# Kernel optimization log

Hardware: AMD Instinct MI355X
Metric: run time of the kernel (lower is better)

Reference implementation:

```python
import jax, jax.numpy as jnp
import numpy as np

CHUNK = 64
L2_EPS = 1e-6
RMS_EPS = 1e-5


def _silu(x):
    return x * jax.nn.sigmoid(x)


def _causal_shared_conv(x, w):
    # x: [B,T,C]; w: [K] single kernel shared across all channels (depthwise).
    K = w.shape[0]
    T = x.shape[1]
    xp = jnp.pad(x, ((0, 0), (K - 1, 0), (0, 0)))
    out = w[0] * xp[:, 0:T, :]
    for j in range(1, K):  # K=4, tiny fixed loop
        out = out + w[j] * xp[:, j:j + T, :]
    return out


def _l2norm(x):
    return x * jax.lax.rsqrt(jnp.sum(x * x, axis=-1, keepdims=True) + L2_EPS)


def _delta_rule_chunk(q, k, v, beta, chunk=CHUNK):
    # q,k: [B,H,T,dk]; v: [B,H,T,dv]; beta: [B,H,T]
    B, H, T, dk = q.shape
    dv = v.shape[-1]
    q = q * (dk ** -0.5)
    nC = T // chunk
    q = q.reshape(B, H, nC, chunk, dk)
    k = k.reshape(B, H, nC, chunk, dk)
    v = v.reshape(B, H, nC, chunk, dv)
    beta = beta.reshape(B, H, nC, chunk)
    k_beta = k * beta[..., None]
    v_beta = v * beta[..., None]
    # UT transform: invert the unit-lower-triangular (I + stril(K_beta K^T))
    A = jnp.einsum('bhncd,bhnmd->bhncm', k_beta, k)  # [B,H,nC,C,C]
    stril = jnp.tril(jnp.ones((chunk, chunk), bool), -1)
    M = jnp.where(stril, A, 0.0) + jnp.eye(chunk, dtype=q.dtype)
    u = jax.scipy.linalg.solve_triangular(M, v_beta, lower=True)  # T @ (beta*v)
    w = jax.scipy.linalg.solve_triangular(M, k_beta, lower=True)  # T @ (beta*k)
    tril_incl = jnp.tril(jnp.ones((chunk, chunk), bool))

    def step(S, inp):
        q_i, k_i, u_i, w_i = inp  # [B,H,C,d*]
        u_i = u_i - jnp.einsum('bhcd,bhde->bhce', w_i, S)
        attn = jnp.where(tril_incl, jnp.einsum('bhcd,bhmd->bhcm', q_i, k_i), 0.0)
        o_i = jnp.einsum('bhcd,bhde->bhce', q_i, S) + jnp.einsum('bhcm,bhme->bhce', attn, u_i)
        S = S + jnp.einsum('bhcd,bhce->bhde', k_i, u_i)
        return S, o_i

    xs = tuple(jnp.moveaxis(t, 2, 0) for t in (q, k, u, w))
    S0 = jnp.zeros((B, H, dk, dv), q.dtype)
    _, o = jax.lax.scan(step, S0, xs)  # o: [nC,B,H,C,dv]
    return jnp.moveaxis(o, 0, 2).reshape(B, H, T, dv)


def setup_inputs() -> dict:
    key = jax.random.key(0)
    ks = jax.random.split(key, 10)
    B, T, D, H = 2, 4096, 2048, 16
    sc = 0.02
    return {
        'x': jax.random.normal(ks[0], (B, T, D), jnp.float32),
        'Wq': jax.random.normal(ks[1], (D, D), jnp.float32) * sc,
        'Wk': jax.random.normal(ks[2], (D, D), jnp.float32) * sc,
        'Wv': jax.random.normal(ks[3], (D, D), jnp.float32) * sc,
        'Wb': jax.random.normal(ks[4], (D, H), jnp.float32) * sc,
        'Wo': jax.random.normal(ks[5], (D, D), jnp.float32) * sc,
        'conv_q': jax.random.normal(ks[6], (4,), jnp.float32) * 0.5,
        'conv_k': jax.random.normal(ks[7], (4,), jnp.float32) * 0.5,
        'conv_v': jax.random.normal(ks[8], (4,), jnp.float32) * 0.5,
        'onorm_w': jnp.ones((D // H,), jnp.float32),
    }


def reference(x, Wq, Wk, Wv, Wb, Wo, conv_q, conv_k, conv_v, onorm_w):
    B, T, D = x.shape
    H = Wb.shape[1]
    dk = Wq.shape[1] // H
    dv = Wv.shape[1] // H
    # projections + shared-kernel causal short conv (silu activation)
    q = _silu(_causal_shared_conv(x @ Wq, conv_q))
    k = _silu(_causal_shared_conv(x @ Wk, conv_k))
    v = _silu(_causal_shared_conv(x @ Wv, conv_v))
    beta = jax.nn.sigmoid(x @ Wb)  # [B,T,H]
    # split heads -> [B,H,T,d]
    qh = _l2norm(q.reshape(B, T, H, dk)).transpose(0, 2, 1, 3)
    kh = _l2norm(k.reshape(B, T, H, dk)).transpose(0, 2, 1, 3)
    vh = v.reshape(B, T, H, dv).transpose(0, 2, 1, 3)
    o = _delta_rule_chunk(qh, kh, vh, beta.transpose(0, 2, 1))  # [B,H,T,dv]
    o = o.transpose(0, 2, 1, 3)  # [B,T,H,dv]
    # per-head RMSNorm over head_v_dim
    o = o * jax.lax.rsqrt(jnp.mean(o * o, axis=-1, keepdims=True) + RMS_EPS) * onorm_w
    return o.reshape(B, T, H * dv) @ Wo
```

## Files before the change

### kernel.cpp

```cpp
#include <hip/hip_runtime.h>
#include <math.h>

#define B_ 2
#define T_ 4096
#define D_ 2048
#define H_ 16
#define DK 128
#define DV 128
#define CH 64
#define M_ (B_ * T_)
#define NCH (T_ / CH)

typedef __attribute__((ext_vector_type(8))) short bfrag;
typedef __attribute__((ext_vector_type(4))) float ffrag;
typedef __attribute__((ext_vector_type(8))) unsigned short u16x8;
typedef unsigned short us;

#define MFMA __builtin_amdgcn_mfma_f32_16x16x32_bf16

__device__ inline us f2bf(float f) {
  union { float f; unsigned u; } v; v.f = f;
  unsigned r = v.u + 0x7fffu + ((v.u >> 16) & 1u);
  return (us)(r >> 16);
}
__device__ inline float bf2f(us u) {
  union { unsigned u; float f; } v; v.u = ((unsigned)u) << 16;
  return v.f;
}

__device__ inline void gl_lds16(const us* g, us* l) {
  __builtin_amdgcn_global_load_lds(
      (const __attribute__((address_space(1))) void*)g,
      (__attribute__((address_space(3))) void*)l, 16, 0, 0);
}

__global__ __launch_bounds__(256) void to_bf16(const float* __restrict__ in,
                                               us* __restrict__ out) {
  const size_t i = ((size_t)blockIdx.x * 256 + threadIdx.x) * 8;
  const float4 a = *reinterpret_cast<const float4*>(in + i);
  const float4 b = *reinterpret_cast<const float4*>(in + i + 4);
  ushort4 o0, o1;
  o0.x = f2bf(a.x); o0.y = f2bf(a.y); o0.z = f2bf(a.z); o0.w = f2bf(a.w);
  o1.x = f2bf(b.x); o1.y = f2bf(b.y); o1.z = f2bf(b.z); o1.w = f2bf(b.w);
  *reinterpret_cast<ushort4*>(out + i) = o0;
  *reinterpret_cast<ushort4*>(out + i + 4) = o1;
}

__global__ __launch_bounds__(256) void beta_sigmoid(const float* __restrict__ x,
                                                    const float* __restrict__ Wb,
                                                    float* __restrict__ betaT) {
  const int t = threadIdx.x;
  const int m = blockIdx.x * 4 + (t >> 6);
  const int l = t & 63;
  const int c = l & 15;
  const int s = l >> 4;
  const float* xr = x + (size_t)m * D_;
  const int kb = s * (D_ / 4);
  float acc = 0.f;
  for (int k = 0; k < D_ / 4; ++k)
    acc = fmaf(xr[kb + k], Wb[(size_t)(kb + k) * H_ + c], acc);
  acc += __shfl_xor(acc, 16);
  acc += __shfl_xor(acc, 32);
  if (l < 16) {
    const int b = m >> 12, tt = m & (T_ - 1);
    betaT[((size_t)(b * H_ + c)) * T_ + tt] = 1.f / (1.f + expf(-acc));
  }
}

__global__ __launch_bounds__(256) void wtrans(const float* __restrict__ W,
                                              us* __restrict__ Wt) {
  __shared__ float tile[64][68];
  const int k0 = blockIdx.y * 64, n0 = blockIdx.x * 64;
  const int lr = threadIdx.x >> 4, lc = (threadIdx.x & 15) * 4;
#pragma unroll
  for (int p = 0; p < 4; ++p) {
    const int r = lr + p * 16;
    *reinterpret_cast<float4*>(&tile[r][lc]) =
        *reinterpret_cast<const float4*>(&W[(size_t)(k0 + r) * D_ + n0 + lc]);
  }
  __syncthreads();
#pragma unroll
  for (int p = 0; p < 4; ++p) {
    const int r = lr + p * 16;
    ushort4 o;
    o.x = f2bf(tile[lc + 0][r]); o.y = f2bf(tile[lc + 1][r]);
    o.z = f2bf(tile[lc + 2][r]); o.w = f2bf(tile[lc + 3][r]);
    *reinterpret_cast<ushort4*>(&Wt[(size_t)(n0 + r) * D_ + k0 + lc]) = o;
  }
}

template <bool OUTF32>
__global__ __launch_bounds__(512, 2) void gemm256(const us* __restrict__ A,
                                                  const us* __restrict__ Bt,
                                                  void* __restrict__ Cp,
                                                  int M, int N, int K) {
  __shared__ __align__(16) us lds[2][2][2][256 * 32];
  const int t = threadIdx.x, l = t & 63, w = t >> 6;
  const int wm = w >> 2, wn = w & 3;
  const int fr = l & 15, hi = l >> 4;
  const int sx = 8 * (hi ^ ((fr >> 1) & 3));

  const int m0 = blockIdx.y * 256;
  const int n0 = blockIdx.x * 256;

  const int srow = t >> 2;
  const int scol = 8 * ((t & 3) ^ ((t >> 3) & 3));
  const us* Ab = A + (size_t)(m0 + srow) * K + scol;
  const us* Bb = Bt + (size_t)(n0 + srow) * K + scol;

  ffrag acc[8][4];
#pragma unroll
  for (int mi = 0; mi < 8; ++mi)
#pragma unroll
    for (int ni = 0; ni < 4; ++ni)
#pragma unroll
      for (int e = 0; e < 4; ++e) acc[mi][ni][e] = 0.f;

#define STG_A(bf, kk, kt)                                                      \
  do {                                                                         \
    gl_lds16(Ab + (size_t)(kt) * 64 + (kk) * 32, &lds[bf][0][kk][t * 8]);      \
    gl_lds16(Ab + (size_t)128 * K + (size_t)(kt) * 64 + (kk) * 32,             \
             &lds[bf][0][kk][4096 + t * 8]);                                   \
  } while (0)
#define STG_B(bf, kk, kt)                                                      \
  do {                                                                         \
    gl_lds16(Bb + (size_t)(kt) * 64 + (kk) * 32, &lds[bf][1][kk][t * 8]);      \
    gl_lds16(Bb + (size_t)128 * K + (size_t)(kt) * 64 + (kk) * 32,             \
             &lds[bf][1][kk][4096 + t * 8]);                                   \
  } while (0)

  const int NT = K >> 6;
  STG_A(0, 0, 0); STG_B(0, 0, 0); STG_A(0, 1, 0); STG_B(0, 1, 0);
  asm volatile("s_waitcnt vmcnt(4)" ::: "memory");
  __builtin_amdgcn_s_barrier();
  __builtin_amdgcn_sched_barrier(0);

  const int arow = wm * 128 + fr;
  const int brow = wn * 64 + fr;

#pragma unroll 1
  for (int kt = 0; kt < NT; ++kt) {
    const int cur = kt & 1, oth = cur ^ 1;
    const bool pf = (kt + 1 < NT);
    bfrag af4[4], bf4[4];

    {
      const us* pa = &lds[cur][0][0][0];
      const us* pb = &lds[cur][1][0][0];
#pragma unroll
      for (int ni = 0; ni < 4; ++ni)
        bf4[ni] = *reinterpret_cast<const bfrag*>(pb + (brow + ni * 16) * 32 + sx);
#pragma unroll
      for (int mi = 0; mi < 4; ++mi)
        af4[mi] = *reinterpret_cast<const bfrag*>(pa + (arow + mi * 16) * 32 + sx);
      if (pf) STG_A(oth, 0, kt + 1);
      __builtin_amdgcn_s_setprio(1);
#pragma unroll
      for (int mi = 0; mi < 4; ++mi)
#pragma unroll
        for (int ni = 0; ni < 4; ++ni)
          acc[mi][ni] = MFMA(af4[mi], bf4[ni], acc[mi][ni], 0, 0, 0);
      __builtin_amdgcn_s_setprio(0);
#pragma unroll
      for (int mi = 0; mi < 4; ++mi)
        af4[mi] = *reinterpret_cast<const bfrag*>(pa + (arow + 64 + mi * 16) * 32 + sx);
      if (pf) STG_B(oth, 0, kt + 1);
      __builtin_amdgcn_s_setprio(1);
#pragma unroll
      for (int mi = 0; mi < 4; ++mi)
#pragma unroll
        for (int ni = 0; ni < 4; ++ni)
          acc[mi + 4][ni] = MFMA(af4[mi], bf4[ni], acc[mi + 4][ni], 0, 0, 0);
      __builtin_amdgcn_s_setprio(0);
    }
    if (pf) asm volatile("s_waitcnt vmcnt(4)" ::: "memory");
    else    asm volatile("s_waitcnt vmcnt(0)" ::: "memory");
    __builtin_amdgcn_s_barrier();
    __builtin_amdgcn_sched_barrier(0);

    {
      const us* pa = &lds[cur][0][1][0];
      const us* pb = &lds[cur][1][1][0];
#pragma unroll
      for (int ni = 0; ni < 4; ++ni)
        bf4[ni] = *reinterpret_cast<const bfrag*>(pb + (brow + ni * 16) * 32 + sx);
#pragma unroll
      for (int mi = 0; mi < 4; ++mi)
        af4[mi] = *reinterpret_cast<const bfrag*>(pa + (arow + mi * 16) * 32 + sx);
      if (pf) STG_A(oth, 1, kt + 1);
      __builtin_amdgcn_s_setprio(1);
#pragma unroll
      for (int mi = 0; mi < 4; ++mi)
#pragma unroll
        for (int ni = 0; ni < 4; ++ni)
          acc[mi][ni] = MFMA(af4[mi], bf4[ni], acc[mi][ni], 0, 0, 0);
      __builtin_amdgcn_s_setprio(0);
#pragma unroll
      for (int mi = 0; mi < 4; ++mi)
        af4[mi] = *reinterpret_cast<const bfrag*>(pa + (arow + 64 + mi * 16) * 32 + sx);
      if (pf) STG_B(oth, 1, kt + 1);
      __builtin_amdgcn_s_setprio(1);
#pragma unroll
      for (int mi = 0; mi < 4; ++mi)
#pragma unroll
        for (int ni = 0; ni < 4; ++ni)
          acc[mi + 4][ni] = MFMA(af4[mi], bf4[ni], acc[mi + 4][ni], 0, 0, 0);
      __builtin_amdgcn_s_setprio(0);
    }
    if (pf) asm volatile("s_waitcnt vmcnt(4)" ::: "memory");
    else    asm volatile("s_waitcnt vmcnt(0)" ::: "memory");
    __builtin_amdgcn_s_barrier();
    __builtin_amdgcn_sched_barrier(0);
  }
#undef STG_A
#undef STG_B

  const int crow = m0 + wm * 128 + hi * 4;
  const int ccol = n0 + wn * 64 + fr;
#pragma unroll
  for (int mi = 0; mi < 8; ++mi)
#pragma unroll
    for (int ni = 0; ni < 4; ++ni)
#pragma unroll
      for (int j = 0; j < 4; ++j) {
        const size_t idx = (size_t)(crow + mi * 16 + j) * N + ccol + ni * 16;
        if constexpr (OUTF32) ((float*)Cp)[idx] = acc[mi][ni][j];
        else ((us*)Cp)[idx] = f2bf(acc[mi][ni][j]);
      }
}

__device__ inline void conv_body(const us* __restrict__ in, const float* cw,
                                 int bt, int d0, int mode, float v[8]) {
  const int tb = bt & (T_ - 1);
  const us* row = in + (size_t)bt * D_ + d0;
#pragma unroll
  for (int j = 0; j < 8; ++j) v[j] = 0.f;
#pragma unroll
  for (int j = 0; j < 4; ++j) {
    if (tb >= j) {
      const us* rp = row - (size_t)(j * D_);
      const ushort4 a = *reinterpret_cast<const ushort4*>(rp);
      const ushort4 b = *reinterpret_cast<const ushort4*>(rp + 4);
      const float wj = cw[3 - j];
      v[0] = fmaf(wj, bf2f(a.x), v[0]); v[1] = fmaf(wj, bf2f(a.y), v[1]);
      v[2] = fmaf(wj, bf2f(a.z), v[2]); v[3] = fmaf(wj, bf2f(a.w), v[3]);
      v[4] = fmaf(wj, bf2f(b.x), v[4]); v[5] = fmaf(wj, bf2f(b.y), v[5]);
      v[6] = fmaf(wj, bf2f(b.z), v[6]); v[7] = fmaf(wj, bf2f(b.w), v[7]);
    }
  }
#pragma unroll
  for (int j = 0; j < 8; ++j) v[j] = v[j] / (1.f + expf(-v[j]));
  if (mode) {
    float ss = 0.f;
#pragma unroll
    for (int j = 0; j < 8; ++j) ss = fmaf(v[j], v[j], ss);
    ss += __shfl_xor(ss, 1);
    ss += __shfl_xor(ss, 2);
    ss += __shfl_xor(ss, 4);
    ss += __shfl_xor(ss, 8);
    float sc = rsqrtf(ss + 1e-6f);
    if (mode == 2) sc *= 0.08838834764831845f;
#pragma unroll
    for (int j = 0; j < 8; ++j) v[j] *= sc;
  }
}

__global__ __launch_bounds__(256) void conv_silu_plain(const us* __restrict__ in,
                                                       const float* __restrict__ cw,
                                                       us* __restrict__ out) {
  const int bt = blockIdx.x, d0 = threadIdx.x * 8;
  float v[8];
  conv_body(in, cw, bt, d0, 0, v);
  ushort4 o0, o1;
  o0.x = f2bf(v[0]); o0.y = f2bf(v[1]); o0.z = f2bf(v[2]); o0.w = f2bf(v[3]);
  o1.x = f2bf(v[4]); o1.y = f2bf(v[5]); o1.z = f2bf(v[6]); o1.w = f2bf(v[7]);
  us* op = out + (size_t)bt * D_ + d0;
  *reinterpret_cast<ushort4*>(op) = o0;
  *reinterpret_cast<ushort4*>(op + 4) = o1;
}

__global__ __launch_bounds__(256) void conv_silu_chunk(const us* __restrict__ in,
                                                       const float* __restrict__ cw,
                                                       us* __restrict__ out,
                                                       int mode) {
  const int bt = blockIdx.x, d0 = threadIdx.x * 8;
  float v[8];
  conv_body(in, cw, bt, d0, mode, v);
  const int b = bt >> 12, tt = bt & (T_ - 1);
  const int cid = tt >> 6, r = tt & 63;
  const int h = d0 >> 7, g = (d0 & 127) >> 3;
  us* dst = out + ((size_t)((b * H_ + h) * NCH + cid)) * (CH * DK) +
            r * 128 + ((g ^ (r & 15)) * 8);
  ushort4 o0, o1;
  o0.x = f2bf(v[0]); o0.y = f2bf(v[1]); o0.z = f2bf(v[2]); o0.w = f2bf(v[3]);
  o1.x = f2bf(v[4]); o1.y = f2bf(v[5]); o1.z = f2bf(v[6]); o1.w = f2bf(v[7]);
  *reinterpret_cast<ushort4*>(dst) = o0;
  *reinterpret_cast<ushort4*>(dst + 4) = o1;
}

__device__ inline void prod_step(float* Tf, const float* Am, float* xbuf,
                                 int r, int c, int I, int J,
                                 int nk, int K0, int K1, int K2) {
  float X = 0.f;
  const int Ks[3] = {K0, K1, K2};
  for (int kk = 0; kk < nk; ++kk) {
    const int K = Ks[kk];
    const float* amrow = Am + (16 * I + r) * 72 + 16 * K;
    const float* tcol = Tf + (16 * K) * 68 + 16 * J + c;
#pragma unroll
    for (int m = 0; m < 16; ++m) X = fmaf(amrow[m], tcol[m * 68], X);
  }
  __syncthreads();
  xbuf[r * 17 + c] = X;
  __syncthreads();
  float s = 0.f;
  const float* trow = Tf + (16 * I + r) * 68 + 16 * I;
#pragma unroll
  for (int m = 0; m < 16; ++m) s = fmaf(trow[m], xbuf[m * 17 + c], s);
  Tf[(16 * I + r) * 68 + 16 * J + c] = -s;
  __syncthreads();
}

__global__ __launch_bounds__(256, 2) void delta_prep(const us* __restrict__ qch,
                                                     const us* __restrict__ kch,
                                                     const float* __restrict__ betaT,
                                                     us* __restrict__ v_uv,
                                                     us* __restrict__ Wout,
                                                     us* __restrict__ kTout,
                                                     us* __restrict__ Aout) {
  __shared__ __align__(16) unsigned char lds[72000];
  us*    ks    = (us*)(lds);
  us*    Tb    = (us*)(lds);
  float* Am    = (float*)(lds + 16384);
  us*    vTb   = (us*)(lds + 16384);
  float* Tf    = (float*)(lds + 34816);
  us*    atst  = (us*)(lds + 34816);
  us*    Wst   = (us*)(lds + 34816);
  us*    kTb   = (us*)(lds + 52224);
  us*    UVst  = (us*)(lds + 52224);
  float* betac = (float*)(lds + 70656);
  float* xbuf  = (float*)(lds + 70912);

  const int t = threadIdx.x, w = t >> 6, l = t & 63;
  const int rr = l & 15, hi = l >> 4;
  const int bx = blockIdx.x;
  const int bh = bx >> 6, cid = bx & 63;
  const int b = bh >> 4, h = bh & 15;
  const size_t rowbase = ((size_t)b * T_ + (size_t)cid * CH) * D_ + (size_t)h * DK;
  const size_t cbase = (size_t)bx * (CH * DK);
  const size_t abase = (size_t)bx * (CH * CH);

  {
    const us* kg = kch + cbase;
#pragma unroll
    for (int p = 0; p < 4; ++p)
      gl_lds16(kg + p * 2048 + t * 8, ks + p * 2048 + t * 8);
    const float4 z = make_float4(0.f, 0.f, 0.f, 0.f);
    *reinterpret_cast<float4*>(atst + t * 16) = z;
    *reinterpret_cast<float4*>(atst + t * 16 + 8) = z;
    if (t < 64) betac[t] = betaT[(size_t)bh * T_ + cid * CH + t];
  }
  __syncthreads();

  {
    bfrag qf[4], kf[4];
#pragma unroll
    for (int k4 = 0; k4 < 4; ++k4) {
      const int go = ((4 * k4 + hi) ^ rr) * 8;
      qf[k4] = *reinterpret_cast<const bfrag*>(qch + cbase + (16 * w + rr) * 128 + go);
      kf[k4] = *reinterpret_cast<const bfrag*>(ks + (16 * w + rr) * 128 + go);
    }
    for (int jt = 0; jt <= w; ++jt) {
      ffrag accA = {0.f, 0.f, 0.f, 0.f}, accQ = {0.f, 0.f, 0.f, 0.f};
#pragma unroll
      for (int k4 = 0; k4 < 4; ++k4) {
        const bfrag bfr = *reinterpret_cast<const bfrag*>(
            ks + (16 * jt + rr) * 128 + (((4 * k4 + hi) ^ rr) * 8));
        accA = MFMA(kf[k4], bfr, accA, 0, 0, 0);
        accQ = MFMA(qf[k4], bfr, accQ, 0, 0, 0);
      }
#pragma unroll
      for (int j4 = 0; j4 < 4; ++j4) {
        const int i = 16 * w + 4 * hi + j4, j = 16 * jt + rr;
        Am[i * 72 + j] = (j < i) ? betac[i] * accA[j4] : 0.f;
        if (j <= i)
          atst[i * 64 + (((j >> 3) ^ (i & 7)) * 8) + (j & 7)] = f2bf(accQ[j4]);
      }
    }
    const int r = t & 63, part = t >> 6;
#pragma unroll
    for (int gi = 0; gi < 4; ++gi) {
      const int g = 4 * part + gi;
      const u16x8 kv = *reinterpret_cast<const u16x8*>(ks + r * 128 + ((g ^ (r & 15)) * 8));
#pragma unroll
      for (int j = 0; j < 8; ++j) kTb[(g * 8 + j) * 72 + r] = kv[j];
    }
  }
  __syncthreads();

  {
#pragma unroll
    for (int p = 0; p < 2; ++p) {
      const int unit = t + p * 256;
      *reinterpret_cast<u16x8*>(Aout + abase + unit * 8) =
          *reinterpret_cast<const u16x8*>(atst + unit * 8);
    }
#pragma unroll
    for (int p = 0; p < 4; ++p) {
      const int unit = t + p * 256;
      const int d = unit >> 3, sg = unit & 7;
      *reinterpret_cast<u16x8*>(kTout + cbase + unit * 8) =
          *reinterpret_cast<const u16x8*>(kTb + d * 72 + ((sg ^ (d & 7)) * 8));
    }
  }
  __syncthreads();
  for (int i = t; i < 64 * 68; i += 256) Tf[i] = 0.f;
  __syncthreads();

  if (t < 64) {
    const int blk = t >> 4, j = t & 15, bd = blk * 16;
    Tf[(bd + j) * 68 + bd + j] = 1.f;
    for (int i = j + 1; i < 16; ++i) {
      float s = 0.f;
      for (int m = j; m < i; ++m)
        s = fmaf(Am[(bd + i) * 72 + bd + m], Tf[(bd + m) * 68 + bd + j], s);
      Tf[(bd + i) * 68 + bd + j] = -s;
    }
  }
  __syncthreads();

  {
    const int r = t >> 4, c = t & 15;
    prod_step(Tf, Am, xbuf, r, c, 1, 0, 1, 0, 0, 0);
    prod_step(Tf, Am, xbuf, r, c, 2, 0, 2, 0, 1, 0);
    prod_step(Tf, Am, xbuf, r, c, 3, 0, 3, 0, 1, 2);
    prod_step(Tf, Am, xbuf, r, c, 2, 1, 1, 1, 0, 0);
    prod_step(Tf, Am, xbuf, r, c, 3, 1, 2, 1, 2, 0);
    prod_step(Tf, Am, xbuf, r, c, 3, 2, 1, 2, 0, 0);
  }

  {
    const int vr = t >> 2, vp = t & 3;
    u16x8 vv[4];
#pragma unroll
    for (int g = 0; g < 4; ++g)
      vv[g] = *reinterpret_cast<const u16x8*>(v_uv + rowbase + (size_t)vr * D_ +
                                              vp * 32 + g * 8);
    const int ti = t >> 2, tg = t & 3;
    u16x8 w0, w1;
#pragma unroll
    for (int jj = 0; jj < 8; ++jj) {
      const int j0 = tg * 16 + jj, j1 = j0 + 8;
      w0[jj] = f2bf(Tf[ti * 68 + j0] * betac[j0]);
      w1[jj] = f2bf(Tf[ti * 68 + j1] * betac[j1]);
    }
    *reinterpret_cast<u16x8*>(Tb + ti * 72 + tg * 16) = w0;
    *reinterpret_cast<u16x8*>(Tb + ti * 72 + tg * 16 + 8) = w1;
#pragma unroll
    for (int g = 0; g < 4; ++g)
#pragma unroll
      for (int j = 0; j < 8; ++j)
        vTb[(vp * 32 + g * 8 + j) * 72 + vr] = vv[g][j];
  }
  __syncthreads();

  {
    bfrag ta[2];
#pragma unroll
    for (int k2 = 0; k2 < 2; ++k2)
      ta[k2] = *reinterpret_cast<const bfrag*>(Tb + (16 * w + rr) * 72 + 32 * k2 + 8 * hi);
#pragma unroll
    for (int dt = 0; dt < 8; ++dt) {
      ffrag acc = {0.f, 0.f, 0.f, 0.f};
#pragma unroll
      for (int k2 = 0; k2 < 2; ++k2) {
        const bfrag bfr = *reinterpret_cast<const bfrag*>(
            kTb + (16 * dt + rr) * 72 + 32 * k2 + 8 * hi);
        acc = MFMA(ta[k2], bfr, acc, 0, 0, 0);
      }
#pragma unroll
      for (int j4 = 0; j4 < 4; ++j4) {
        const int i = 16 * w + 4 * hi + j4, d = 16 * dt + rr;
        Wst[i * 128 + (((d >> 3) ^ (i & 15)) * 8) + (d & 7)] = f2bf(-acc[j4]);
      }
    }
  }
  __syncthreads();

  {
    bfrag ta[2];
#pragma unroll
    for (int k2 = 0; k2 < 2; ++k2)
      ta[k2] = *reinterpret_cast<const bfrag*>(Tb + (16 * w + rr) * 72 + 32 * k2 + 8 * hi);
#pragma unroll
    for (int et = 0; et < 8; ++et) {
      ffrag acc = {0.f, 0.f, 0.f, 0.f};
#pragma unroll
      for (int k2 = 0; k2 < 2; ++k2) {
        const bfrag bfr = *reinterpret_cast<const bfrag*>(
            vTb + (16 * et + rr) * 72 + 32 * k2 + 8 * hi);
        acc = MFMA(ta[k2], bfr, acc, 0, 0, 0);
      }
#pragma unroll
      for (int j4 = 0; j4 < 4; ++j4)
        UVst[(16 * w + 4 * hi + j4) * 128 + 16 * et + rr] = f2bf(acc[j4]);
    }
#pragma unroll
    for (int p = 0; p < 4; ++p) {
      const int unit = t + p * 256;
      *reinterpret_cast<u16x8*>(Wout + cbase + unit * 8) =
          *reinterpret_cast<const u16x8*>(Wst + unit * 8);
    }
  }
  __syncthreads();

#pragma unroll
  for (int p = 0; p < 4; ++p) {
    const int unit = t + p * 256;
    const int r = unit >> 4, g = unit & 15;
    *reinterpret_cast<u16x8*>(v_uv + rowbase + (size_t)r * D_ + g * 8) =
        *reinterpret_cast<const u16x8*>(UVst + r * 128 + g * 8);
  }
}

__global__ __launch_bounds__(512, 1) void delta_seq(const us* __restrict__ qch,
                                                    const us* __restrict__ Wch,
                                                    const us* __restrict__ kTch,
                                                    const us* __restrict__ atch,
                                                    us* __restrict__ uv_o) {
  __shared__ __align__(16) us qs[2][CH * DK];
  __shared__ __align__(16) us Ws[2][CH * DK];
  __shared__ __align__(16) us kTs[2][DK * CH];
  __shared__ __align__(16) us ats[2][CH * CH];
  __shared__ __align__(16) us uvs[2][CH * 16];
  __shared__ __align__(16) us Sb[2][16 * 136];
  __shared__ __align__(16) us ub[CH * 18];
  __shared__ __align__(16) us ob[CH * 18];

  const int t = threadIdx.x, l = t & 63, w = t >> 6;
  const int bx = blockIdx.x;
  const int vs = bx >> 5, bh = bx & 31;
  const int b = bh >> 4, h = bh & 15;
  const int rr = l & 15, hi = l >> 4;
  const int w2 = w & 3;

  ffrag sacc[2];
#pragma unroll
  for (int t2 = 0; t2 < 2; ++t2)
#pragma unroll
    for (int j = 0; j < 4; ++j) sacc[t2][j] = 0.f;

  for (int i = t; i < 16 * 136; i += 512) Sb[0][i] = 0;

  const size_t cbQ = (size_t)(bh * NCH) * (CH * DK);
  const size_t cbA = (size_t)(bh * NCH) * (CH * CH);
  const size_t rowbase0 = ((size_t)b * T_) * D_ + (size_t)h * DK + vs * 16;

#define STAGE(buf, cid)                                                        \
  do {                                                                         \
    const us* qg = qch + cbQ + (size_t)(cid) * (CH * DK);                      \
    const us* Wg = Wch + cbQ + (size_t)(cid) * (CH * DK);                      \
    const us* kg = kTch + cbQ + (size_t)(cid) * (CH * DK);                     \
    const us* ag = atch + cbA + (size_t)(cid) * (CH * CH);                     \
    gl_lds16(qg + t * 8, &qs[buf][t * 8]);                                     \
    gl_lds16(qg + 4096 + t * 8, &qs[buf][4096 + t * 8]);                       \
    gl_lds16(Wg + t * 8, &Ws[buf][t * 8]);                                     \
    gl_lds16(Wg + 4096 + t * 8, &Ws[buf][4096 + t * 8]);                       \
    gl_lds16(kg + t * 8, &kTs[buf][t * 8]);                                    \
    gl_lds16(kg + 4096 + t * 8, &kTs[buf][4096 + t * 8]);                      \
    gl_lds16(ag + t * 8, &ats[buf][t * 8]);                                    \
    if (t < 128)                                                               \
      gl_lds16(uv_o + rowbase0 + (size_t)((cid) * CH + (t >> 1)) * D_ + (t & 1) * 8, \
               &uvs[buf][t * 8]);                                              \
  } while (0)

  STAGE(0, 0);
  asm volatile("s_waitcnt vmcnt(0) lgkmcnt(0)" ::: "memory");
  __builtin_amdgcn_s_barrier();
  __builtin_amdgcn_sched_barrier(0);

  for (int cid = 0; cid < NCH; ++cid) {
    const int cur = cid & 1;

    if (cid > 0 && t < 128) {
      const u16x8 ov = *reinterpret_cast<const u16x8*>(&ob[(t >> 1) * 18 + (t & 1) * 8]);
      *reinterpret_cast<u16x8*>(uv_o + rowbase0 +
          (size_t)((cid - 1) * CH + (t >> 1)) * D_ + (t & 1) * 8) = ov;
    }
    if (cid + 1 < NCH) STAGE(cur ^ 1, cid + 1);

    bfrag sbf[4];
#pragma unroll
    for (int ks = 0; ks < 4; ++ks)
      sbf[ks] = *reinterpret_cast<const bfrag*>(&Sb[cur][rr * 136 + ks * 32 + hi * 8]);

    ffrag acc4;
    if (w < 4) {
#pragma unroll
      for (int j = 0; j < 4; ++j)
        acc4[j] = bf2f(uvs[cur][(16 * w + 4 * hi + j) * 16 + rr]);
#pragma unroll
      for (int ks = 0; ks < 4; ++ks) {
        const bfrag af = *reinterpret_cast<const bfrag*>(
            &Ws[cur][(16 * w + rr) * 128 + (((4 * ks + hi) ^ rr) * 8)]);
        acc4 = MFMA(af, sbf[ks], acc4, 0, 0, 0);
      }
#pragma unroll
      for (int j = 0; j < 4; ++j)
        ub[(16 * w + 4 * hi + j) * 18 + rr] = f2bf(acc4[j]);
    } else {
#pragma unroll
      for (int j = 0; j < 4; ++j) acc4[j] = 0.f;
#pragma unroll
      for (int ks = 0; ks < 4; ++ks) {
        const bfrag af = *reinterpret_cast<const bfrag*>(
            &qs[cur][(16 * w2 + rr) * 128 + (((4 * ks + hi) ^ rr) * 8)]);
        acc4 = MFMA(af, sbf[ks], acc4, 0, 0, 0);
      }
    }
    asm volatile("s_waitcnt lgkmcnt(0)" ::: "memory");
    __builtin_amdgcn_s_barrier();
    __builtin_amdgcn_sched_barrier(0);

    if (w < 4) {
      bfrag ubf[2];
#pragma unroll
      for (int ks = 0; ks < 2; ++ks)
#pragma unroll
        for (int j = 0; j < 8; ++j)
          ubf[ks][j] = (short)ub[(32 * ks + 8 * hi + j) * 18 + rr];
#pragma unroll
      for (int t2 = 0; t2 < 2; ++t2) {
        const int tile = 2 * w + t2;
#pragma unroll
        for (int ks = 0; ks < 2; ++ks) {
          const bfrag af = *reinterpret_cast<const bfrag*>(
              &kTs[cur][(16 * tile + rr) * 64 + (((4 * ks + hi) ^ (rr & 7)) * 8)]);
          sacc[t2] = MFMA(af, ubf[ks], sacc[t2], 0, 0, 0);
        }
        ushort4 sw;
        sw.x = f2bf(sacc[t2][0]); sw.y = f2bf(sacc[t2][1]);
        sw.z = f2bf(sacc[t2][2]); sw.w = f2bf(sacc[t2][3]);
        *reinterpret_cast<ushort4*>(&Sb[cur ^ 1][rr * 136 + 16 * tile + 4 * hi]) = sw;
      }
    } else {
      const int nks = (w2 < 2) ? 1 : 2;
      for (int ks = 0; ks < nks; ++ks) {
        bfrag ubf;
#pragma unroll
        for (int j = 0; j < 8; ++j)
          ubf[j] = (short)ub[(32 * ks + 8 * hi + j) * 18 + rr];
        const bfrag af = *reinterpret_cast<const bfrag*>(
            &ats[cur][(16 * w2 + rr) * 64 + (((4 * ks + hi) ^ (rr & 7)) * 8)]);
        acc4 = MFMA(af, ubf, acc4, 0, 0, 0);
      }
#pragma unroll
      for (int j = 0; j < 4; ++j)
        ob[(16 * w2 + 4 * hi + j) * 18 + rr] = f2bf(acc4[j]);
    }
    asm volatile("s_waitcnt vmcnt(0) lgkmcnt(0)" ::: "memory");
    __builtin_amdgcn_s_barrier();
    __builtin_amdgcn_sched_barrier(0);
  }
#undef STAGE

  if (t < 128) {
    const u16x8 ov = *reinterpret_cast<const u16x8*>(&ob[(t >> 1) * 18 + (t & 1) * 8]);
    *reinterpret_cast<u16x8*>(uv_o + rowbase0 +
        (size_t)((NCH - 1) * CH + (t >> 1)) * D_ + (t & 1) * 8) = ov;
  }
}

__global__ __launch_bounds__(256) void rms_onorm_bf16(const us* __restrict__ in,
                                                      const float* __restrict__ w,
                                                      us* __restrict__ out) {
  const int bt = blockIdx.x;
  const int d0 = threadIdx.x * 8;
  const us* p = in + (size_t)bt * D_ + d0;
  const ushort4 a = *reinterpret_cast<const ushort4*>(p);
  const ushort4 b = *reinterpret_cast<const ushort4*>(p + 4);
  float v[8] = {bf2f(a.x), bf2f(a.y), bf2f(a.z), bf2f(a.w),
                bf2f(b.x), bf2f(b.y), bf2f(b.z), bf2f(b.w)};
  float ss = 0.f;
#pragma unroll
  for (int j = 0; j < 8; ++j) ss = fmaf(v[j], v[j], ss);
  ss += __shfl_xor(ss, 1);
  ss += __shfl_xor(ss, 2);
  ss += __shfl_xor(ss, 4);
  ss += __shfl_xor(ss, 8);
  const float sc = rsqrtf(ss * (1.0f / 128.0f) + 1e-5f);
  const int hd = d0 & 127;
  ushort4 o0, o1;
  o0.x = f2bf(v[0] * sc * w[hd + 0]); o0.y = f2bf(v[1] * sc * w[hd + 1]);
  o0.z = f2bf(v[2] * sc * w[hd + 2]); o0.w = f2bf(v[3] * sc * w[hd + 3]);
  o1.x = f2bf(v[4] * sc * w[hd + 4]); o1.y = f2bf(v[5] * sc * w[hd + 5]);
  o1.z = f2bf(v[6] * sc * w[hd + 6]); o1.w = f2bf(v[7] * sc * w[hd + 7]);
  us* op = out + (size_t)bt * D_ + d0;
  *reinterpret_cast<ushort4*>(op) = o0;
  *reinterpret_cast<ushort4*>(op + 4) = o1;
}

extern "C" void kernel_launch(void* const* d_in, const int* in_sizes, int n_in,
                              void* d_out, int out_size, void* d_ws, size_t ws_size,
                              hipStream_t stream) {
  const float* x  = (const float*)d_in[0];
  const float* Wq = (const float*)d_in[1];
  const float* Wk = (const float*)d_in[2];
  const float* Wv = (const float*)d_in[3];
  const float* Wb = (const float*)d_in[4];
  const float* Wo = (const float*)d_in[5];
  const float* cq = (const float*)d_in[6];
  const float* ck = (const float*)d_in[7];
  const float* cv = (const float*)d_in[8];
  const float* ow = (const float*)d_in[9];
  float* out = (float*)d_out;

  const size_t NE = (size_t)M_ * D_;
  us* ws   = (us*)d_ws;
  us* gout = ws;
  us* qch  = ws + NE;
  us* kch  = ws + 2 * NE;
  us* Wch  = ws + 3 * NE;
  us* kTch = ws + 4 * NE;
  us* wt   = ws + 5 * NE;
  us* attb = gout;
  float* betaT = (float*)(ws + 5 * NE + (size_t)D_ * D_);
  us* xb = (us*)d_out;
  us* vb = xb + NE;

  dim3 gg(D_ / 256, M_ / 256);
  dim3 wg(D_ / 64, D_ / 64);

  to_bf16<<<NE / 2048, 256, 0, stream>>>(x, xb);

  wtrans<<<wg, 256, 0, stream>>>(Wv, wt);
  gemm256<false><<<gg, 512, 0, stream>>>(xb, wt, gout, M_, D_, D_);
  conv_silu_plain<<<M_, 256, 0, stream>>>(gout, cv, vb);

  wtrans<<<wg, 256, 0, stream>>>(Wq, wt);
  gemm256<false><<<gg, 512, 0, stream>>>(xb, wt, gout, M_, D_, D_);
  conv_silu_chunk<<<M_, 256, 0, stream>>>(gout, cq, qch, 2);

  wtrans<<<wg, 256, 0, stream>>>(Wk, wt);
  gemm256<false><<<gg, 512, 0, stream>>>(xb, wt, gout, M_, D_, D_);
  conv_silu_chunk<<<M_, 256, 0, stream>>>(gout, ck, kch, 1);

  beta_sigmoid<<<M_ / 4, 256, 0, stream>>>(x, Wb, betaT);

  delta_prep<<<32 * NCH, 256, 0, stream>>>(qch, kch, betaT, vb, Wch, kTch, attb);
  delta_seq<<<256, 512, 0, stream>>>(qch, Wch, kTch, attb, vb);

  rms_onorm_bf16<<<M_, 256, 0, stream>>>(vb, ow, kTch);

  wtrans<<<wg, 256, 0, stream>>>(Wo, wt);
  gemm256<true><<<gg, 512, 0, stream>>>(kTch, wt, out, M_, D_, D_);
}
```

Before: 636.6 us.

## Triple-buffer delta_seq staging and load kT fragments directly into registers

The sequential delta-rule kernel now keeps three LDS buffers and prefetches two chunks ahead instead of one. It replaces the full vmcnt(0) drain with per-wave partial waits, so loads for later chunks stay in flight across barriers. The kT operand no longer goes through LDS and is read from global memory straight into registers at the top of each iteration. The uv loads and stores are split into 4-byte pieces so all 512 threads take part. The hand-counted vmcnt values must match the exact number of outstanding loads per wave, which makes the code fragile.

```diff
diff --git a/kernel.cpp b/kernel.cpp
--- a/kernel.cpp
+++ b/kernel.cpp
@@ -32,6 +32,11 @@
   __builtin_amdgcn_global_load_lds(
       (const __attribute__((address_space(1))) void*)g,
       (__attribute__((address_space(3))) void*)l, 16, 0, 0);
+}
+__device__ inline void gl_lds4(const us* g, us* l) {
+  __builtin_amdgcn_global_load_lds(
+      (const __attribute__((address_space(1))) void*)g,
+      (__attribute__((address_space(3))) void*)l, 4, 0, 0);
 }
 
 __global__ __launch_bounds__(256) void to_bf16(const float* __restrict__ in,
@@ -528,11 +533,10 @@
                                                     const us* __restrict__ kTch,
                                                     const us* __restrict__ atch,
                                                     us* __restrict__ uv_o) {
-  __shared__ __align__(16) us qs[2][CH * DK];
-  __shared__ __align__(16) us Ws[2][CH * DK];
-  __shared__ __align__(16) us kTs[2][DK * CH];
-  __shared__ __align__(16) us ats[2][CH * CH];
-  __shared__ __align__(16) us uvs[2][CH * 16];
+  __shared__ __align__(16) us qs[3][CH * DK];
+  __shared__ __align__(16) us Ws[3][CH * DK];
+  __shared__ __align__(16) us ats[3][CH * CH];
+  __shared__ __align__(16) us uvs[3][CH * 16];
   __shared__ __align__(16) us Sb[2][16 * 136];
   __shared__ __align__(16) us ub[CH * 18];
   __shared__ __align__(16) us ob[CH * 18];
@@ -560,34 +564,43 @@
   do {                                                                         \
     const us* qg = qch + cbQ + (size_t)(cid) * (CH * DK);                      \
     const us* Wg = Wch + cbQ + (size_t)(cid) * (CH * DK);                      \
-    const us* kg = kTch + cbQ + (size_t)(cid) * (CH * DK);                     \
     const us* ag = atch + cbA + (size_t)(cid) * (CH * CH);                     \
     gl_lds16(qg + t * 8, &qs[buf][t * 8]);                                     \
     gl_lds16(qg + 4096 + t * 8, &qs[buf][4096 + t * 8]);                       \
     gl_lds16(Wg + t * 8, &Ws[buf][t * 8]);                                     \
     gl_lds16(Wg + 4096 + t * 8, &Ws[buf][4096 + t * 8]);                       \
-    gl_lds16(kg + t * 8, &kTs[buf][t * 8]);                                    \
-    gl_lds16(kg + 4096 + t * 8, &kTs[buf][4096 + t * 8]);                      \
     gl_lds16(ag + t * 8, &ats[buf][t * 8]);                                    \
-    if (t < 128)                                                               \
-      gl_lds16(uv_o + rowbase0 + (size_t)((cid) * CH + (t >> 1)) * D_ + (t & 1) * 8, \
-               &uvs[buf][t * 8]);                                              \
+    gl_lds4(uv_o + rowbase0 + (size_t)((cid) * CH + (t >> 3)) * D_ + (t & 7) * 2, \
+            &uvs[buf][t * 2]);                                                 \
   } while (0)
 
   STAGE(0, 0);
-  asm volatile("s_waitcnt vmcnt(0) lgkmcnt(0)" ::: "memory");
+  STAGE(1, 1);
+  asm volatile("s_waitcnt vmcnt(6) lgkmcnt(0)" ::: "memory");
   __builtin_amdgcn_s_barrier();
   __builtin_amdgcn_sched_barrier(0);
 
   for (int cid = 0; cid < NCH; ++cid) {
+    const int cur3 = cid % 3;
     const int cur = cid & 1;
 
-    if (cid > 0 && t < 128) {
-      const u16x8 ov = *reinterpret_cast<const u16x8*>(&ob[(t >> 1) * 18 + (t & 1) * 8]);
-      *reinterpret_cast<u16x8*>(uv_o + rowbase0 +
-          (size_t)((cid - 1) * CH + (t >> 1)) * D_ + (t & 1) * 8) = ov;
-    }
-    if (cid + 1 < NCH) STAGE(cur ^ 1, cid + 1);
+    if (cid > 0) {
+      const ushort2 ov = *reinterpret_cast<const ushort2*>(&ob[(t >> 3) * 18 + (t & 7) * 2]);
+      *reinterpret_cast<ushort2*>(uv_o + rowbase0 +
+          (size_t)((cid - 1) * CH + (t >> 3)) * D_ + (t & 7) * 2) = ov;
+    }
+    u16x8 ktf[4];
+    if (w < 4) {
+      const us* kg = kTch + cbQ + (size_t)cid * (CH * DK);
+#pragma unroll
+      for (int t2 = 0; t2 < 2; ++t2)
+#pragma unroll
+        for (int ks = 0; ks < 2; ++ks)
+          ktf[t2 * 2 + ks] = *reinterpret_cast<const u16x8*>(
+              kg + (16 * (2 * w + t2) + rr) * 64 + (((4 * ks + hi) ^ (rr & 7)) * 8));
+    }
+    __builtin_amdgcn_sched_barrier(0);
+    if (cid + 2 < NCH) STAGE((cid + 2) % 3, cid + 2);
 
     bfrag sbf[4];
 #pragma unroll
@@ -598,11 +611,11 @@
     if (w < 4) {
 #pragma unroll
       for (int j = 0; j < 4; ++j)
-        acc4[j] = bf2f(uvs[cur][(16 * w + 4 * hi + j) * 16 + rr]);
+        acc4[j] = bf2f(uvs[cur3][(16 * w + 4 * hi + j) * 16 + rr]);
 #pragma unroll
       for (int ks = 0; ks < 4; ++ks) {
         const bfrag af = *reinterpret_cast<const bfrag*>(
-            &Ws[cur][(16 * w + rr) * 128 + (((4 * ks + hi) ^ rr) * 8)]);
+            &Ws[cur3][(16 * w + rr) * 128 + (((4 * ks + hi) ^ rr) * 8)]);
         acc4 = MFMA(af, sbf[ks], acc4, 0, 0, 0);
       }
 #pragma unroll
@@ -614,7 +627,7 @@
 #pragma unroll
       for (int ks = 0; ks < 4; ++ks) {
         const bfrag af = *reinterpret_cast<const bfrag*>(
-            &qs[cur][(16 * w2 + rr) * 128 + (((4 * ks + hi) ^ rr) * 8)]);
+            &qs[cur3][(16 * w2 + rr) * 128 + (((4 * ks + hi) ^ rr) * 8)]);
         acc4 = MFMA(af, sbf[ks], acc4, 0, 0, 0);
       }
     }
@@ -634,8 +647,7 @@
         const int tile = 2 * w + t2;
 #pragma unroll
         for (int ks = 0; ks < 2; ++ks) {
-          const bfrag af = *reinterpret_cast<const bfrag*>(
-              &kTs[cur][(16 * tile + rr) * 64 + (((4 * ks + hi) ^ (rr & 7)) * 8)]);
+          const bfrag af = *reinterpret_cast<const bfrag*>(&ktf[t2 * 2 + ks]);
           sacc[t2] = MFMA(af, ubf[ks], sacc[t2], 0, 0, 0);
         }
         ushort4 sw;
@@ -651,23 +663,34 @@
         for (int j = 0; j < 8; ++j)
           ubf[j] = (short)ub[(32 * ks + 8 * hi + j) * 18 + rr];
         const bfrag af = *reinterpret_cast<const bfrag*>(
-            &ats[cur][(16 * w2 + rr) * 64 + (((4 * ks + hi) ^ (rr & 7)) * 8)]);
+            &ats[cur3][(16 * w2 + rr) * 64 + (((4 * ks + hi) ^ (rr & 7)) * 8)]);
         acc4 = MFMA(af, ubf, acc4, 0, 0, 0);
       }
 #pragma unroll
       for (int j = 0; j < 4; ++j)
         ob[(16 * w2 + 4 * hi + j) * 18 + rr] = f2bf(acc4[j]);
     }
-    asm volatile("s_waitcnt vmcnt(0) lgkmcnt(0)" ::: "memory");
+
+    if (cid == NCH - 1) {
+      asm volatile("s_waitcnt vmcnt(0) lgkmcnt(0)" ::: "memory");
+    } else if (w < 4) {
+      if (cid == 0)            asm volatile("s_waitcnt vmcnt(10) lgkmcnt(0)" ::: "memory");
+      else if (cid == NCH - 2) asm volatile("s_waitcnt vmcnt(5) lgkmcnt(0)" ::: "memory");
+      else                     asm volatile("s_waitcnt vmcnt(11) lgkmcnt(0)" ::: "memory");
+    } else {
+      if (cid == 0)            asm volatile("s_waitcnt vmcnt(6) lgkmcnt(0)" ::: "memory");
+      else if (cid == NCH - 2) asm volatile("s_waitcnt vmcnt(1) lgkmcnt(0)" ::: "memory");
+      else                     asm volatile("s_waitcnt vmcnt(7) lgkmcnt(0)" ::: "memory");
+    }
     __builtin_amdgcn_s_barrier();
     __builtin_amdgcn_sched_barrier(0);
   }
 #undef STAGE
 
-  if (t < 128) {
-    const u16x8 ov = *reinterpret_cast<const u16x8*>(&ob[(t >> 1) * 18 + (t & 1) * 8]);
-    *reinterpret_cast<u16x8*>(uv_o + rowbase0 +
-        (size_t)((NCH - 1) * CH + (t >> 1)) * D_ + (t & 1) * 8) = ov;
+  {
+    const ushort2 ov = *reinterpret_cast<const ushort2*>(&ob[(t >> 3) * 18 + (t & 7) * 2]);
+    *reinterpret_cast<ushort2*>(uv_o + rowbase0 +
+        (size_t)((NCH - 1) * CH + (t >> 3)) * D_ + (t & 7) * 2) = ov;
   }
 }
 
```

Measured after the change: 639.8 us. Within noise of the previous version (+0.5%).

## Replace double-buffered GEMM K-loop with four-slot ring prefetching three steps ahead

Applied to the files above, without the earlier changes.

The bf16 GEMM's K loop moves from a double buffer of 64-wide K tiles (each split into two 32-wide halves with interleaved staging) to a 4-slot LDS ring of 32-wide K tiles. Loads are issued three tiles ahead, with one barrier per 32-wide step. This hides more global-load latency behind the MFMA work. In exchange, launch bounds drop from 2 to 1 blocks per SM, and all 8 A fragments are now held in registers at once, which raises register pressure and cuts occupancy.

```diff
diff --git a/kernel.cpp b/kernel.cpp
--- a/kernel.cpp
+++ b/kernel.cpp
@@ -90,11 +90,11 @@
 }
 
 template <bool OUTF32>
-__global__ __launch_bounds__(512, 2) void gemm256(const us* __restrict__ A,
+__global__ __launch_bounds__(512, 1) void gemm256(const us* __restrict__ A,
                                                   const us* __restrict__ Bt,
                                                   void* __restrict__ Cp,
                                                   int M, int N, int K) {
-  __shared__ __align__(16) us lds[2][2][2][256 * 32];
+  __shared__ __align__(16) us ring[4][2][256 * 32];
   const int t = threadIdx.x, l = t & 63, w = t >> 6;
   const int wm = w >> 2, wn = w & 3;
   const int fr = l & 15, hi = l >> 4;
@@ -116,22 +116,17 @@
 #pragma unroll
       for (int e = 0; e < 4; ++e) acc[mi][ni][e] = 0.f;
 
-#define STG_A(bf, kk, kt)                                                      \
+#define STAGE(slot, kt)                                                        \
   do {                                                                         \
-    gl_lds16(Ab + (size_t)(kt) * 64 + (kk) * 32, &lds[bf][0][kk][t * 8]);      \
-    gl_lds16(Ab + (size_t)128 * K + (size_t)(kt) * 64 + (kk) * 32,             \
-             &lds[bf][0][kk][4096 + t * 8]);                                   \
+    gl_lds16(Ab + (size_t)(kt) * 32, &ring[slot][0][t * 8]);                   \
+    gl_lds16(Ab + (size_t)128 * K + (size_t)(kt) * 32, &ring[slot][0][4096 + t * 8]); \
+    gl_lds16(Bb + (size_t)(kt) * 32, &ring[slot][1][t * 8]);                   \
+    gl_lds16(Bb + (size_t)128 * K + (size_t)(kt) * 32, &ring[slot][1][4096 + t * 8]); \
   } while (0)
-#define STG_B(bf, kk, kt)                                                      \
-  do {                                                                         \
-    gl_lds16(Bb + (size_t)(kt) * 64 + (kk) * 32, &lds[bf][1][kk][t * 8]);      \
-    gl_lds16(Bb + (size_t)128 * K + (size_t)(kt) * 64 + (kk) * 32,             \
-             &lds[bf][1][kk][4096 + t * 8]);                                   \
-  } while (0)
-
-  const int NT = K >> 6;
-  STG_A(0, 0, 0); STG_B(0, 0, 0); STG_A(0, 1, 0); STG_B(0, 1, 0);
-  asm volatile("s_waitcnt vmcnt(4)" ::: "memory");
+
+  const int NT = K >> 5;
+  STAGE(0, 0); STAGE(1, 1); STAGE(2, 2);
+  asm volatile("s_waitcnt vmcnt(8)" ::: "memory");
   __builtin_amdgcn_s_barrier();
   __builtin_amdgcn_sched_barrier(0);
 
@@ -140,80 +135,35 @@
 
 #pragma unroll 1
   for (int kt = 0; kt < NT; ++kt) {
-    const int cur = kt & 1, oth = cur ^ 1;
-    const bool pf = (kt + 1 < NT);
-    bfrag af4[4], bf4[4];
-
-    {
-      const us* pa = &lds[cur][0][0][0];
-      const us* pb = &lds[cur][1][0][0];
+    const int cur = kt & 3;
+    const us* pa = &ring[cur][0][0];
+    const us* pb = &ring[cur][1][0];
+
+    bfrag bf4[4], af[8];
+#pragma unroll
+    for (int ni = 0; ni < 4; ++ni)
+      bf4[ni] = *reinterpret_cast<const bfrag*>(pb + (brow + ni * 16) * 32 + sx);
+#pragma unroll
+    for (int mi = 0; mi < 8; ++mi)
+      af[mi] = *reinterpret_cast<const bfrag*>(pa + (arow + mi * 16) * 32 + sx);
+
+    if (kt + 3 < NT) STAGE((kt + 3) & 3, kt + 3);
+
+    __builtin_amdgcn_s_setprio(1);
+#pragma unroll
+    for (int mi = 0; mi < 8; ++mi)
 #pragma unroll
       for (int ni = 0; ni < 4; ++ni)
-        bf4[ni] = *reinterpret_cast<const bfrag*>(pb + (brow + ni * 16) * 32 + sx);
-#pragma unroll
-      for (int mi = 0; mi < 4; ++mi)
-        af4[mi] = *reinterpret_cast<const bfrag*>(pa + (arow + mi * 16) * 32 + sx);
-      if (pf) STG_A(oth, 0, kt + 1);
-      __builtin_amdgcn_s_setprio(1);
-#pragma unroll
-      for (int mi = 0; mi < 4; ++mi)
-#pragma unroll
-        for (int ni = 0; ni < 4; ++ni)
-          acc[mi][ni] = MFMA(af4[mi], bf4[ni], acc[mi][ni], 0, 0, 0);
-      __builtin_amdgcn_s_setprio(0);
-#pragma unroll
-      for (int mi = 0; mi < 4; ++mi)
-        af4[mi] = *reinterpret_cast<const bfrag*>(pa + (arow + 64 + mi * 16) * 32 + sx);
-      if (pf) STG_B(oth, 0, kt + 1);
-      __builtin_amdgcn_s_setprio(1);
-#pragma unroll
-      for (int mi = 0; mi < 4; ++mi)
-#pragma unroll
-        for (int ni = 0; ni < 4; ++ni)
-          acc[mi + 4][ni] = MFMA(af4[mi], bf4[ni], acc[mi + 4][ni], 0, 0, 0);
-      __builtin_amdgcn_s_setprio(0);
-    }
-    if (pf) asm volatile("s_waitcnt vmcnt(4)" ::: "memory");
-    else    asm volatile("s_waitcnt vmcnt(0)" ::: "memory");
+        acc[mi][ni] = MFMA(af[mi], bf4[ni], acc[mi][ni], 0, 0, 0);
+    __builtin_amdgcn_s_setprio(0);
+
+    if (kt + 3 < NT)      asm volatile("s_waitcnt vmcnt(8)" ::: "memory");
+    else if (kt + 2 < NT) asm volatile("s_waitcnt vmcnt(4)" ::: "memory");
+    else if (kt + 1 < NT) asm volatile("s_waitcnt vmcnt(0)" ::: "memory");
     __builtin_amdgcn_s_barrier();
     __builtin_amdgcn_sched_barrier(0);
-
-    {
-      const us* pa = &lds[cur][0][1][0];
-      const us* pb = &lds[cur][1][1][0];
-#pragma unroll
-      for (int ni = 0; ni < 4; ++ni)
-        bf4[ni] = *reinterpret_cast<const bfrag*>(pb + (brow + ni * 16) * 32 + sx);
-#pragma unroll
-      for (int mi = 0; mi < 4; ++mi)
-        af4[mi] = *reinterpret_cast<const bfrag*>(pa + (arow + mi * 16) * 32 + sx);
-      if (pf) STG_A(oth, 1, kt + 1);
-      __builtin_amdgcn_s_setprio(1);
-#pragma unroll
-      for (int mi = 0; mi < 4; ++mi)
-#pragma unroll
-        for (int ni = 0; ni < 4; ++ni)
-          acc[mi][ni] = MFMA(af4[mi], bf4[ni], acc[mi][ni], 0, 0, 0);
-      __builtin_amdgcn_s_setprio(0);
-#pragma unroll
-      for (int mi = 0; mi < 4; ++mi)
-        af4[mi] = *reinterpret_cast<const bfrag*>(pa + (arow + 64 + mi * 16) * 32 + sx);
-      if (pf) STG_B(oth, 1, kt + 1);
-      __builtin_amdgcn_s_setprio(1);
-#pragma unroll
-      for (int mi = 0; mi < 4; ++mi)
-#pragma unroll
-        for (int ni = 0; ni < 4; ++ni)
-          acc[mi + 4][ni] = MFMA(af4[mi], bf4[ni], acc[mi + 4][ni], 0, 0, 0);
-      __builtin_amdgcn_s_setprio(0);
-    }
-    if (pf) asm volatile("s_waitcnt vmcnt(4)" ::: "memory");
-    else    asm volatile("s_waitcnt vmcnt(0)" ::: "memory");
-    __builtin_amdgcn_s_barrier();
-    __builtin_amdgcn_sched_barrier(0);
-  }
-#undef STG_A
-#undef STG_B
+  }
+#undef STAGE
 
   const int crow = m0 + wm * 128 + hi * 4;
   const int ccol = n0 + wn * 64 + fr;
```

Result: no change. 642.4 us (+0.9%).
